# Performance work log

Measured on AMD Instinct MI355X. Metric: run time of the kernel, lower is better.

## Reference

```python
import jax, jax.numpy as jnp
import numpy as np

D_MODEL = 1024
N_HEADS = 16
D_K = D_MODEL // N_HEADS


def setup_inputs() -> dict:
    key = jax.random.key(0)
    ks = jax.random.split(key, 6)
    B, S = 4, 2048
    x = jax.random.normal(ks[0], (B, S, D_MODEL), dtype=jnp.float32)
    # nn.Linear weights are [out, in]; kept in that layout, applied as x @ W.T
    lim = 1.0 / np.sqrt(D_MODEL)
    w_q = jax.random.uniform(ks[1], (D_MODEL, D_MODEL), jnp.float32, -lim, lim)
    w_k = jax.random.uniform(ks[2], (D_MODEL, D_MODEL), jnp.float32, -lim, lim)
    w_v = jax.random.uniform(ks[3], (D_MODEL, D_MODEL), jnp.float32, -lim, lim)
    w_o = jax.random.uniform(ks[4], (D_MODEL, D_MODEL), jnp.float32, -lim, lim)
    b_o = jax.random.uniform(ks[5], (D_MODEL,), jnp.float32, -lim, lim)
    return {"x": x, "w_q": w_q, "w_k": w_k, "w_v": w_v, "w_o": w_o, "b_o": b_o}


def reference(x, w_q, w_k, w_v, w_o, b_o):
    B, S, _ = x.shape
    scale = 1.0 / np.sqrt(D_K).astype(np.float32)

    def split_heads(t):  # [B,S,D] -> [B,H,S,d_k]
        return t.reshape(B, S, N_HEADS, D_K).transpose(0, 2, 1, 3)

    q = split_heads(x @ w_q.T)
    k = split_heads(x @ w_k.T)
    v = split_heads(x @ w_v.T)

    scores = jnp.einsum('bhqd,bhkd->bhqk', q, k) * scale
    causal = jnp.tril(jnp.ones((S, S), dtype=bool))
    scores = jnp.where(causal[None, None], scores, -jnp.inf)
    attn = jax.nn.softmax(scores, axis=-1)  # dropout p=0 -> identity
    out = jnp.einsum('bhqk,bhkd->bhqd', attn, v)
    out = out.transpose(0, 2, 1, 3).reshape(B, S, D_MODEL)
    return out @ w_o.T + b_o
```

## Files before the change

kernel.cpp:

```cpp
#include <hip/hip_runtime.h>

typedef unsigned short ushort_t;
typedef __attribute__((ext_vector_type(8))) short short8;
typedef __attribute__((ext_vector_type(4))) float floatx4;


__device__ __forceinline__ ushort_t f2bf(float f) {
    unsigned int u = __float_as_uint(f);
    u = (u + 0x7FFFu + ((u >> 16) & 1u)) >> 16;
    return (ushort_t)u;
}

typedef __attribute__((address_space(1))) void gls_g;
typedef __attribute__((address_space(3))) void gls_l;

__device__ __forceinline__ void async_copy16(const ushort_t* g, ushort_t* l) {
    __builtin_amdgcn_global_load_lds((gls_g*)g, (gls_l*)l, 16, 0, 0);
}

__device__ __forceinline__ floatx4 mfma16(short8 a, short8 b, floatx4 c) {
    return __builtin_amdgcn_mfma_f32_16x16x32_bf16(a, b, c, 0, 0, 0);
}


__global__ __launch_bounds__(256) void conv_bf16(const float* __restrict__ in,
                                                 ushort_t* __restrict__ out, int n) {
    int i = (blockIdx.x * 256 + threadIdx.x) * 4;
    if (i < n) {
        float4 f = *(const float4*)(in + i);
        ushort4 o;
        o.x = f2bf(f.x); o.y = f2bf(f.y); o.z = f2bf(f.z); o.w = f2bf(f.w);
        *(ushort4*)(out + i) = o;
    }
}


template<int BF16_OUT>
__global__ __launch_bounds__(256, 2) void gemm_nt(const ushort_t* __restrict__ A,
                                                  const ushort_t* __restrict__ B,
                                                  void* __restrict__ Cv,
                                                  const float* __restrict__ bias,
                                                  int M, int N, int K, int ldc) {
    __shared__ ushort_t lA[128 * 32];
    __shared__ ushort_t lB[128 * 32];
    const int tid  = threadIdx.x;
    const int wave = tid >> 6, lane = tid & 63;
    const int quad = lane >> 4, l15 = lane & 15;
    const int wr = (wave >> 1) * 64;
    const int wc = (wave & 1) * 64;
    const size_t bm = blockIdx.y, bn = blockIdx.x;

    const ushort_t* Ab = A + bm * 128 * (size_t)K;
    const ushort_t* Bb = B + bn * 128 * (size_t)K;

    floatx4 acc[4][4];
#pragma unroll
    for (int i = 0; i < 4; ++i)
#pragma unroll
        for (int j = 0; j < 4; ++j) acc[i][j] = (floatx4){0.f, 0.f, 0.f, 0.f};

    for (int kt = 0; kt < K; kt += 32) {
        __syncthreads();
#pragma unroll
        for (int i = 0; i < 2; ++i) {
            const int li  = i * 256 + tid;
            const int row = li >> 2;
            const int ko  = (li & 3) * 8;
            async_copy16(Ab + (size_t)row * K + kt + ko, &lA[i * 2048 + wave * 512]);
            async_copy16(Bb + (size_t)row * K + kt + ko, &lB[i * 2048 + wave * 512]);
        }
        __syncthreads();

        short8 af[4], bf[4];
#pragma unroll
        for (int mt = 0; mt < 4; ++mt)
            af[mt] = *(const short8*)&lA[(wr + mt * 16 + l15) * 32 + quad * 8];
#pragma unroll
        for (int nt = 0; nt < 4; ++nt)
            bf[nt] = *(const short8*)&lB[(wc + nt * 16 + l15) * 32 + quad * 8];
#pragma unroll
        for (int mt = 0; mt < 4; ++mt)
#pragma unroll
            for (int nt = 0; nt < 4; ++nt)
                acc[mt][nt] = mfma16(af[mt], bf[nt], acc[mt][nt]);
    }

#pragma unroll
    for (int mt = 0; mt < 4; ++mt)
#pragma unroll
        for (int nt = 0; nt < 4; ++nt)
#pragma unroll
            for (int r = 0; r < 4; ++r) {
                const size_t m = bm * 128 + wr + mt * 16 + quad * 4 + r;
                const size_t n = bn * 128 + wc + nt * 16 + l15;
                const float v = acc[mt][nt][r];
                if (BF16_OUT)
                    ((ushort_t*)Cv)[m * (size_t)ldc + n] = f2bf(v);
                else
                    ((float*)Cv)[m * (size_t)ldc + n] = v + bias[n];
            }
}


__global__ __launch_bounds__(256) void transpose_v(const ushort_t* __restrict__ qkv,
                                                   ushort_t* __restrict__ vt) {
    const int bh = blockIdx.y, b = bh >> 4, h = bh & 15;
    const int st = blockIdx.x;
    const int t  = threadIdx.x;
    const int sl  = t >> 2;
    const int dv0 = (t & 3) * 16;
    const int s = st * 64 + sl;
    const ushort_t* src = qkv + (size_t)(b * 2048 + s) * 3072 + 2048 + h * 64 + dv0;
    ushort_t v[16];
    *(uint4*)&v[0] = *(const uint4*)src;
    *(uint4*)&v[8] = *(const uint4*)(src + 8);
    const int s_lo = s & 31;
    const int j = ((s_lo >> 2) & 3) * 8 + ((s_lo >> 4) & 1) * 4 + (s_lo & 3);
    ushort_t* dst = vt + (size_t)(bh * 64) * 2048 + (s & ~31) + j;
#pragma unroll
    for (int i = 0; i < 16; ++i) dst[(size_t)(dv0 + i) * 2048] = v[i];
}


__global__ __launch_bounds__(256, 2) void attn_fwd(const ushort_t* __restrict__ qkv,
                                                   const ushort_t* __restrict__ vt,
                                                   ushort_t* __restrict__ attn) {
    __shared__ ushort_t lK[2][2048];
    __shared__ ushort_t lV[2][2048];
    const int tid = threadIdx.x, wave = tid >> 6, lane = tid & 63;
    const int quad = lane >> 4, l15 = lane & 15;
    const int bh = blockIdx.x & 63;
    const int slot = blockIdx.x >> 6;
    const int b = bh >> 4, h = bh & 15;

    const ushort_t* qb = qkv + (size_t)b * 2048 * 3072 + h * 64;
    const ushort_t* kb = qb + 1024;
    const ushort_t* vb = vt + (size_t)(bh * 64) * 2048;

    const int krow = tid >> 3;
    const ushort_t* ksrc = kb + (size_t)krow * 3072 + ((tid & 7) ^ (krow & 7)) * 8;
    const int vrow = tid >> 2;
    const ushort_t* vsrc = vb + (size_t)vrow * 2048 +
                           ((tid & 3) ^ ((vrow ^ (vrow >> 2)) & 3)) * 8;
    ushort_t* kdst = &lK[0][0] + wave * 512;
    ushort_t* vdst = &lV[0][0] + wave * 512;

    const int vfc = (quad ^ ((l15 ^ (l15 >> 2)) & 3)) * 8;
    const float C = 0.18033688011112042f;

#pragma unroll 1
    for (int phase = 0; phase < 2; ++phase) {
        const int t = phase ? 63 - (slot * 4 + wave) : slot * 4 + wave;
        const int n = phase ? 64 - slot * 4 : slot * 4 + 4;
        const int q0 = t * 32;

        short8 qf[2][2];
#pragma unroll
        for (int mt = 0; mt < 2; ++mt)
#pragma unroll
            for (int ks = 0; ks < 2; ++ks)
                qf[mt][ks] = *(const short8*)(qb +
                    (size_t)(q0 + mt * 16 + l15) * 3072 + ks * 32 + quad * 8);

        floatx4 o[2][4];
        float l[2] = {0.f, 0.f};
#pragma unroll
        for (int mt = 0; mt < 2; ++mt)
#pragma unroll
            for (int d = 0; d < 4; ++d) o[mt][d] = (floatx4){0.f, 0.f, 0.f, 0.f};

        __syncthreads();
        async_copy16(ksrc, kdst);
        async_copy16(vsrc, vdst);

#pragma unroll 1
        for (int ti = 0; ti < n; ++ti) {
            __syncthreads();
            if (ti + 1 < n) {
                const int nb = (ti + 1) & 1;
                async_copy16(ksrc + (size_t)(ti + 1) * 98304, kdst + nb * 2048);
                async_copy16(vsrc + (ti + 1) * 32,            vdst + nb * 2048);
            }
            if (ti <= t) {
                const int buf = ti & 1;
                const ushort_t* Kb = &lK[buf][0];
                const ushort_t* Vb = &lV[buf][0];
                short8 kf[2][2], vf[4];
#pragma unroll
                for (int ksub = 0; ksub < 2; ++ksub)
#pragma unroll
                    for (int ks = 0; ks < 2; ++ks)
                        kf[ksub][ks] = *(const short8*)(Kb + (ksub * 16 + l15) * 64 +
                                           (((ks * 4 + quad) ^ (l15 & 7)) * 8));
#pragma unroll
                for (int d = 0; d < 4; ++d)
                    vf[d] = *(const short8*)(Vb + (d * 16 + l15) * 32 + vfc);

                const bool diag = (ti == t);
#pragma unroll
                for (int mt = 0; mt < 2; ++mt) {
                    const floatx4 z = {0.f, 0.f, 0.f, 0.f};
                    floatx4 s0 = mfma16(kf[0][0], qf[mt][0], z);
                    s0 = mfma16(kf[0][1], qf[mt][1], s0);
                    float p[8];
                    if (mt == 0 && diag) {
#pragma unroll
                        for (int r = 0; r < 4; ++r) {
                            p[r] = __builtin_amdgcn_exp2f(s0[r] * C);
                            if (quad * 4 + r > l15) p[r] = 0.f;
                            p[r + 4] = 0.f;
                        }
                    } else {
                        floatx4 s1 = mfma16(kf[1][0], qf[mt][0], z);
                        s1 = mfma16(kf[1][1], qf[mt][1], s1);
#pragma unroll
                        for (int r = 0; r < 4; ++r) {
                            p[r]     = __builtin_amdgcn_exp2f(s0[r] * C);
                            p[r + 4] = __builtin_amdgcn_exp2f(s1[r] * C);
                        }
                        if (diag) {
#pragma unroll
                            for (int r = 0; r < 4; ++r)
                                if (quad * 4 + r > l15) p[r + 4] = 0.f;
                        }
                    }
                    l[mt] += ((p[0] + p[1]) + (p[2] + p[3])) +
                             ((p[4] + p[5]) + (p[6] + p[7]));

                    union { unsigned u[4]; short8 s8; } pk;
#pragma unroll
                    for (int j = 0; j < 4; ++j)
                        pk.u[j] = __builtin_amdgcn_perm(__float_as_uint(p[2 * j + 1]),
                                                        __float_as_uint(p[2 * j]),
                                                        0x07060302u);
                    const short8 pb = pk.s8;
#pragma unroll
                    for (int d = 0; d < 4; ++d)
                        o[mt][d] = mfma16(vf[d], pb, o[mt][d]);
                }
            }
        }

#pragma unroll
        for (int mt = 0; mt < 2; ++mt) {
            float lt = l[mt];
            lt += __shfl_xor(lt, 16);
            lt += __shfl_xor(lt, 32);
            const float inv = 1.0f / lt;
            ushort_t* orow = attn + (size_t)(b * 2048 + q0 + mt * 16 + l15) * 1024 + h * 64;
#pragma unroll
            for (int d = 0; d < 4; ++d) {
                ushort4 ov;
                ov.x = f2bf(o[mt][d][0] * inv);
                ov.y = f2bf(o[mt][d][1] * inv);
                ov.z = f2bf(o[mt][d][2] * inv);
                ov.w = f2bf(o[mt][d][3] * inv);
                *(ushort4*)(orow + d * 16 + quad * 4) = ov;
            }
        }
    }
}


extern "C" void kernel_launch(void* const* d_in, const int* in_sizes, int n_in,
                              void* d_out, int out_size, void* d_ws, size_t ws_size,
                              hipStream_t stream) {
    const float* x  = (const float*)d_in[0];
    const float* wq = (const float*)d_in[1];
    const float* wk = (const float*)d_in[2];
    const float* wv = (const float*)d_in[3];
    const float* wo = (const float*)d_in[4];
    const float* bo = (const float*)d_in[5];

    char* ws = (char*)d_ws;
    ushort_t* xb   = (ushort_t*)(ws);
    ushort_t* wqkv = (ushort_t*)(ws + 16777216);
    ushort_t* wob  = (ushort_t*)(ws + 23068672);
    ushort_t* qkv  = (ushort_t*)(ws + 25165824);
    ushort_t* vtb  = (ushort_t*)(ws + 75497472);
    ushort_t* attn = xb;
    float* out = (float*)d_out;

    conv_bf16<<<8192, 256, 0, stream>>>(x,  xb,             8388608);
    conv_bf16<<<1024, 256, 0, stream>>>(wq, wqkv,           1048576);
    conv_bf16<<<1024, 256, 0, stream>>>(wk, wqkv + 1048576, 1048576);
    conv_bf16<<<1024, 256, 0, stream>>>(wv, wqkv + 2097152, 1048576);
    conv_bf16<<<1024, 256, 0, stream>>>(wo, wob,            1048576);

    gemm_nt<1><<<dim3(24, 64), 256, 0, stream>>>(xb, wqkv, qkv, nullptr,
                                                 8192, 3072, 1024, 3072);
    transpose_v<<<dim3(32, 64), 256, 0, stream>>>(qkv, vtb);
    attn_fwd<<<512, 256, 0, stream>>>(qkv, vtb, attn);
    gemm_nt<0><<<dim3(8, 64), 256, 0, stream>>>(attn, wob, out, bo,
                                                8192, 1024, 1024, 1024);
}
```

Baseline: 269.4 us.

## Merge bf16 conversion launches and deepen GEMM K-tile with XOR-swizzled LDS

The five fp32-to-bf16 conversion launches become one kernel that picks its source and destination from the block index, which removes four launches. The shared GEMM now stages a 64-wide K slice per iteration instead of 32, halving the number of barrier pairs per tile. It stores the LDS tile with an XOR swizzle on 16-byte chunks to avoid bank conflicts on the wider rows. LDS use doubles to 32 KB per block, which may affect occupancy at two blocks per CU.

```diff
diff --git a/kernel.cpp b/kernel.cpp
--- a/kernel.cpp
+++ b/kernel.cpp
@@ -23,15 +23,30 @@
 }
 
 
-__global__ __launch_bounds__(256) void conv_bf16(const float* __restrict__ in,
-                                                 ushort_t* __restrict__ out, int n) {
-    int i = (blockIdx.x * 256 + threadIdx.x) * 4;
-    if (i < n) {
-        float4 f = *(const float4*)(in + i);
-        ushort4 o;
-        o.x = f2bf(f.x); o.y = f2bf(f.y); o.z = f2bf(f.z); o.w = f2bf(f.w);
-        *(ushort4*)(out + i) = o;
+__global__ __launch_bounds__(256) void conv_all(const float* __restrict__ x,
+                                                const float* __restrict__ wq,
+                                                const float* __restrict__ wk,
+                                                const float* __restrict__ wv,
+                                                const float* __restrict__ wo,
+                                                ushort_t* __restrict__ xb,
+                                                ushort_t* __restrict__ wqkv,
+                                                ushort_t* __restrict__ wob) {
+    const int bid = blockIdx.x;
+    const float* in;
+    ushort_t* out;
+    int blk;
+    if (bid < 8192) { in = x; out = xb; blk = bid; }
+    else {
+        const int g = (bid - 8192) >> 10;
+        blk = (bid - 8192) & 1023;
+        in  = (g == 0) ? wq : (g == 1) ? wk : (g == 2) ? wv : wo;
+        out = (g == 3) ? wob : wqkv + g * 1048576;
     }
+    const int i = (blk * 256 + threadIdx.x) * 4;
+    float4 f = *(const float4*)(in + i);
+    ushort4 o;
+    o.x = f2bf(f.x); o.y = f2bf(f.y); o.z = f2bf(f.z); o.w = f2bf(f.w);
+    *(ushort4*)(out + i) = o;
 }
 
 
@@ -41,8 +56,8 @@
                                                   void* __restrict__ Cv,
                                                   const float* __restrict__ bias,
                                                   int M, int N, int K, int ldc) {
-    __shared__ ushort_t lA[128 * 32];
-    __shared__ ushort_t lB[128 * 32];
+    __shared__ ushort_t lA[128 * 64];
+    __shared__ ushort_t lB[128 * 64];
     const int tid  = threadIdx.x;
     const int wave = tid >> 6, lane = tid & 63;
     const int quad = lane >> 4, l15 = lane & 15;
@@ -53,36 +68,51 @@
     const ushort_t* Ab = A + bm * 128 * (size_t)K;
     const ushort_t* Bb = B + bn * 128 * (size_t)K;
 
+    int srow[4], scol[4];
+#pragma unroll
+    for (int i = 0; i < 4; ++i) {
+        const int li = i * 256 + tid;
+        srow[i] = li >> 3;
+        scol[i] = ((li & 7) ^ (srow[i] & 7)) * 8;
+    }
+
     floatx4 acc[4][4];
 #pragma unroll
     for (int i = 0; i < 4; ++i)
 #pragma unroll
         for (int j = 0; j < 4; ++j) acc[i][j] = (floatx4){0.f, 0.f, 0.f, 0.f};
 
-    for (int kt = 0; kt < K; kt += 32) {
+    for (int kt = 0; kt < K; kt += 64) {
         __syncthreads();
 #pragma unroll
-        for (int i = 0; i < 2; ++i) {
-            const int li  = i * 256 + tid;
-            const int row = li >> 2;
-            const int ko  = (li & 3) * 8;
-            async_copy16(Ab + (size_t)row * K + kt + ko, &lA[i * 2048 + wave * 512]);
-            async_copy16(Bb + (size_t)row * K + kt + ko, &lB[i * 2048 + wave * 512]);
+        for (int i = 0; i < 4; ++i) {
+            async_copy16(Ab + (size_t)srow[i] * K + kt + scol[i],
+                         &lA[i * 2048] + wave * 512);
+            async_copy16(Bb + (size_t)srow[i] * K + kt + scol[i],
+                         &lB[i * 2048] + wave * 512);
         }
         __syncthreads();
 
-        short8 af[4], bf[4];
+        short8 af[4][2], bf[4][2];
 #pragma unroll
         for (int mt = 0; mt < 4; ++mt)
-            af[mt] = *(const short8*)&lA[(wr + mt * 16 + l15) * 32 + quad * 8];
+#pragma unroll
+            for (int ks = 0; ks < 2; ++ks)
+                af[mt][ks] = *(const short8*)&lA[(wr + mt * 16 + l15) * 64 +
+                                                 (((ks * 4 + quad) ^ (l15 & 7)) * 8)];
 #pragma unroll
         for (int nt = 0; nt < 4; ++nt)
-            bf[nt] = *(const short8*)&lB[(wc + nt * 16 + l15) * 32 + quad * 8];
+#pragma unroll
+            for (int ks = 0; ks < 2; ++ks)
+                bf[nt][ks] = *(const short8*)&lB[(wc + nt * 16 + l15) * 64 +
+                                                 (((ks * 4 + quad) ^ (l15 & 7)) * 8)];
 #pragma unroll
         for (int mt = 0; mt < 4; ++mt)
 #pragma unroll
-            for (int nt = 0; nt < 4; ++nt)
-                acc[mt][nt] = mfma16(af[mt], bf[nt], acc[mt][nt]);
+            for (int nt = 0; nt < 4; ++nt) {
+                acc[mt][nt] = mfma16(af[mt][0], bf[nt][0], acc[mt][nt]);
+                acc[mt][nt] = mfma16(af[mt][1], bf[nt][1], acc[mt][nt]);
+            }
     }
 
 #pragma unroll
@@ -281,11 +311,7 @@
     ushort_t* attn = xb;
     float* out = (float*)d_out;
 
-    conv_bf16<<<8192, 256, 0, stream>>>(x,  xb,             8388608);
-    conv_bf16<<<1024, 256, 0, stream>>>(wq, wqkv,           1048576);
-    conv_bf16<<<1024, 256, 0, stream>>>(wk, wqkv + 1048576, 1048576);
-    conv_bf16<<<1024, 256, 0, stream>>>(wv, wqkv + 2097152, 1048576);
-    conv_bf16<<<1024, 256, 0, stream>>>(wo, wob,            1048576);
+    conv_all<<<12288, 256, 0, stream>>>(x, wq, wk, wv, wo, xb, wqkv, wob);
 
     gemm_nt<1><<<dim3(24, 64), 256, 0, stream>>>(xb, wqkv, qkv, nullptr,
                                                  8192, 3072, 1024, 3072);
```

After: 238.1 us. 11.6% less time.
